# Kernel optimization log

Measured on AMD Instinct MI355X. Metric: run time of the kernel, lower is better.

The kernel has to match this reference:

```python
import jax, jax.numpy as jnp
import numpy as np

N_NODES = 10000

def _gcn_norm(edges, n_nodes):
    # PyG GCNConv default: add self-loops, symmetric normalization D^-1/2 A_hat D^-1/2
    src, dst = edges[0], edges[1]
    loop = jnp.arange(n_nodes, dtype=src.dtype)
    src = jnp.concatenate([src, loop])
    dst = jnp.concatenate([dst, loop])
    deg = jax.ops.segment_sum(jnp.ones_like(dst, dtype=jnp.float32), dst, num_segments=n_nodes)
    dinv = jnp.where(deg > 0, jax.lax.rsqrt(deg), 0.0)
    norm = dinv[src] * dinv[dst]  # [E + N]
    return src, dst, norm

def _gcn_layer(x, src, dst, norm, W, b):
    # linear transform, then gather -> weight -> scatter-add aggregation
    x = x @ W  # [N, F]
    msg = x[src] * norm[:, None]  # [E+N, F]
    out = jax.ops.segment_sum(msg, dst, num_segments=x.shape[0])
    return out + b

def setup_inputs() -> dict:
    key = jax.random.key(0)
    k1, k2, k3, k4 = jax.random.split(key, 4)
    d = 128
    E = 640000
    scale = 1.0 / np.sqrt(d)
    return {
        "nodes_embeddings": jax.random.normal(k1, (N_NODES, d), dtype=jnp.float32),
        "edges": jax.random.randint(k2, (2, E), 0, N_NODES, dtype=jnp.int64),
        "W1": jax.random.normal(k3, (d, d), dtype=jnp.float32) * scale,
        "b1": jnp.zeros((d,), dtype=jnp.float32),
        "W2": jax.random.normal(k4, (d, d), dtype=jnp.float32) * scale,
        "b2": jnp.zeros((d,), dtype=jnp.float32),
    }

def reference(nodes_embeddings, edges, W1, b1, W2, b2):
    src, dst, norm = _gcn_norm(edges, nodes_embeddings.shape[0])
    x = _gcn_layer(nodes_embeddings, src, dst, norm, W1, b1)
    x = _gcn_layer(x, src, dst, norm, W2, b2)
    return x
```

## Files before the change

kernel.cpp:

```cpp
#include <hip/hip_runtime.h>
#include <hip/hip_bf16.h>

#define D 128
#define NBINS 157
#define BIN_CAP 5120
#define EPB 4096

__device__ __forceinline__ unsigned rne_bf16(float f) {
    unsigned u = __float_as_uint(f);
    return (u + 0x7FFFu + ((u >> 16) & 1u)) >> 16;
}
__device__ __forceinline__ float bf16_lo(unsigned u) { return __uint_as_float(u << 16); }
__device__ __forceinline__ float bf16_hi(unsigned u) { return __uint_as_float(u & 0xFFFF0000u); }

__global__ __launch_bounds__(512) void fused_gemm_scatter(
        const float* __restrict__ X, const float* __restrict__ W,
        float* __restrict__ Y,
        const int* __restrict__ src, const int* __restrict__ dst,
        int* __restrict__ binTotal, int* __restrict__ binned,
        int E, int N, int gGemm) {
    __shared__ float smem[D * D];
    int tid = threadIdx.x;

    if ((int)blockIdx.x < gGemm) {
        {
            const float4* W4 = (const float4*)W;
            float4* Ws4 = (float4*)smem;
            #pragma unroll
            for (int i = 0; i < 8; ++i)
                Ws4[tid + 512 * i] = W4[tid + 512 * i];
        }
        __syncthreads();
        const float2* Ws2 = (const float2*)smem;
        int col2 = tid & 63;
        int wv   = __builtin_amdgcn_readfirstlane(tid >> 6);
        int row0 = blockIdx.x * 32 + wv * 4;
        if (row0 >= N) return;

        const float4* xr[4];
        #pragma unroll
        for (int r = 0; r < 4; ++r) {
            int rr = row0 + r; if (rr > N - 1) rr = N - 1;
            xr[r] = (const float4*)(X + (size_t)rr * D);
        }
        float accx[4] = {0.f, 0.f, 0.f, 0.f};
        float accy[4] = {0.f, 0.f, 0.f, 0.f};
        #pragma unroll 8
        for (int kb = 0; kb < 32; ++kb) {
            float4 xv[4];
            #pragma unroll
            for (int r = 0; r < 4; ++r) xv[r] = xr[r][kb];
            #pragma unroll
            for (int kk = 0; kk < 4; ++kk) {
                float2 w = Ws2[(4 * kb + kk) * 64 + col2];
                #pragma unroll
                for (int r = 0; r < 4; ++r) {
                    float xs = ((const float*)&xv[r])[kk];
                    accx[r] = fmaf(xs, w.x, accx[r]);
                    accy[r] = fmaf(xs, w.y, accy[r]);
                }
            }
        }
        #pragma unroll
        for (int r = 0; r < 4; ++r) {
            int rr = row0 + r;
            if (rr < N)
                ((float2*)Y)[(size_t)rr * 64 + col2] = make_float2(accx[r], accy[r]);
        }
    } else {
        int* cnt   = (int*)smem;
        int* loff  = cnt + 160;
        int* gbase = cnt + 320;
        int* scur  = cnt + 480;
        int* stage = cnt + 640;
        for (int b = tid; b < NBINS; b += 512) cnt[b] = 0;
        __syncthreads();

        int bid = blockIdx.x - gGemm;
        int base = bid * EPB + tid * 8;
        int s[8], dl[8], bn[8];
        int ne = 0;
        if (base + 8 <= E) {
            const int4* s4 = (const int4*)(src + base);
            const int4* d4 = (const int4*)(dst + base);
            int4 a0 = s4[0], a1 = s4[1], c0 = d4[0], c1 = d4[1];
            int ss[8] = {a0.x, a0.y, a0.z, a0.w, a1.x, a1.y, a1.z, a1.w};
            int dd[8] = {c0.x, c0.y, c0.z, c0.w, c1.x, c1.y, c1.z, c1.w};
            ne = 8;
            #pragma unroll
            for (int i = 0; i < 8; ++i) { s[i] = ss[i]; bn[i] = dd[i] >> 6; dl[i] = dd[i] & 63; }
        } else {
            for (int i = 0; i < 8; ++i) {
                int e = base + i;
                if (e < E) { s[ne] = src[e]; int d = dst[e]; bn[ne] = d >> 6; dl[ne] = d & 63; ++ne; }
            }
        }
        for (int i = 0; i < ne; ++i) atomicAdd(&cnt[bn[i]], 1);
        __syncthreads();

        if (tid < NBINS) gbase[tid] = atomicAdd(&binTotal[tid], cnt[tid]);
        if (tid < 64) {
            int c0 = (3 * tid     < NBINS) ? cnt[3 * tid    ] : 0;
            int c1 = (3 * tid + 1 < NBINS) ? cnt[3 * tid + 1] : 0;
            int c2 = (3 * tid + 2 < NBINS) ? cnt[3 * tid + 2] : 0;
            int tsum = c0 + c1 + c2;
            int incl = tsum;
            #pragma unroll
            for (int off = 1; off < 64; off <<= 1) {
                int t = __shfl_up(incl, off);
                if (tid >= off) incl += t;
            }
            int excl = incl - tsum;
            if (3 * tid     < NBINS) loff[3 * tid    ] = excl;
            if (3 * tid + 1 < NBINS) loff[3 * tid + 1] = excl + c0;
            if (3 * tid + 2 < NBINS) loff[3 * tid + 2] = excl + c0 + c1;
        }
        __syncthreads();
        if (tid < NBINS) scur[tid] = loff[tid];
        __syncthreads();

        for (int i = 0; i < ne; ++i) {
            int p = atomicAdd(&scur[bn[i]], 1);
            stage[p] = s[i] | (dl[i] << 14);
        }
        __syncthreads();

        int wv = tid >> 6, lane = tid & 63;
        for (int b = wv; b < NBINS; b += 8) {
            int n = cnt[b], so = loff[b], go = b * BIN_CAP + gbase[b];
            for (int i = lane; i < n; i += 64) binned[go + i] = stage[so + i];
        }
    }
}

__global__ __launch_bounds__(256) void sort_bins(const int* __restrict__ binTotal,
                                                 const int* __restrict__ binned,
                                                 unsigned short* __restrict__ csr16,
                                                 float* __restrict__ dinv,
                                                 int* __restrict__ nodeStart,
                                                 int* __restrict__ nodeEnd,
                                                 const float* __restrict__ Y,
                                                 unsigned* __restrict__ Zb, int N) {
    __shared__ int h[4][64];
    __shared__ int cur[4][64];
    __shared__ float sdinv[64];
    __shared__ int padTot;
    __shared__ int stage[BIN_CAP];
    int b = blockIdx.x, tid = threadIdx.x;
    int wv = tid >> 6, lane = tid & 63;
    int cntb = binTotal[b];
    h[wv][lane] = 0;
    __syncthreads();
    const int* bp = binned + b * BIN_CAP;
    for (int i = tid; i < cntb; i += 256) atomicAdd(&h[wv][bp[i] >> 14], 1);
    __syncthreads();
    if (tid < 64) {
        int d0 = h[0][tid], d1 = h[1][tid], d2 = h[2][tid], d3 = h[3][tid];
        int deg = d0 + d1 + d2 + d3;
        int pdeg = (deg + 7) & ~7;
        int incl = pdeg;
        #pragma unroll
        for (int off = 1; off < 64; off <<= 1) {
            int t = __shfl_up(incl, off);
            if (tid >= off) incl += t;
        }
        int excl = incl - pdeg;
        cur[0][tid] = excl;
        cur[1][tid] = excl + d0;
        cur[2][tid] = excl + d0 + d1;
        cur[3][tid] = excl + d0 + d1 + d2;
        float dv = rsqrtf((float)(deg + 1));
        sdinv[tid] = dv;
        if (tid == 63) padTot = incl;
        int node = b * 64 + tid;
        if (node < N) {
            dinv[node]      = dv;
            nodeStart[node] = b * BIN_CAP + excl;
            nodeEnd[node]   = b * BIN_CAP + excl + pdeg;
        }
    }
    __syncthreads();
    int cntPad = padTot;
    for (int i = tid; i < cntPad; i += 256) stage[i] = N;
    __syncthreads();
    for (int i = tid; i < cntb; i += 256) {
        int p = bp[i];
        int pos = atomicAdd(&cur[wv][p >> 14], 1);
        stage[pos] = p & 0x3FFF;
    }
    {
        const float4* Y4 = (const float4*)Y;
        uint2* Zb2 = (uint2*)Zb;
        #pragma unroll
        for (int i = 0; i < 8; ++i) {
            int idx = tid + 256 * i;
            int row = idx >> 5, c = idx & 31;
            int node = b * 64 + row;
            if (node < N) {
                float4 v = Y4[(size_t)node * 32 + c];
                float dv = sdinv[row];
                uint2 o;
                o.x = (rne_bf16(v.y * dv) << 16) | rne_bf16(v.x * dv);
                o.y = (rne_bf16(v.w * dv) << 16) | rne_bf16(v.z * dv);
                Zb2[(size_t)node * 32 + c] = o;
            }
        }
    }
    if (b == 0 && tid < 64) Zb[(size_t)N * 64 + tid] = 0u;
    __syncthreads();
    unsigned short* bw = csr16 + b * BIN_CAP;
    for (int i = tid; i < cntPad; i += 256) bw[i] = (unsigned short)stage[i];
}

__global__ __launch_bounds__(256) void gemm_scale(const float* __restrict__ X,
                                                  const float* __restrict__ W,
                                                  const float* __restrict__ dinv,
                                                  unsigned* __restrict__ Zb, int N) {
    __shared__ float Ws[D * D];
    {
        const float4* W4 = (const float4*)W;
        float4* Ws4 = (float4*)Ws;
        #pragma unroll
        for (int i = 0; i < 16; ++i)
            Ws4[threadIdx.x + 256 * i] = W4[threadIdx.x + 256 * i];
    }
    __syncthreads();
    const float2* Ws2 = (const float2*)Ws;
    int col2 = threadIdx.x & 63;
    int wv   = __builtin_amdgcn_readfirstlane(threadIdx.x >> 6);
    int row0 = blockIdx.x * 16 + wv * 4;
    if (row0 >= N) return;

    const float4* xr[4];
    #pragma unroll
    for (int r = 0; r < 4; ++r) {
        int rr = row0 + r; if (rr > N - 1) rr = N - 1;
        xr[r] = (const float4*)(X + (size_t)rr * D);
    }
    float accx[4] = {0.f, 0.f, 0.f, 0.f};
    float accy[4] = {0.f, 0.f, 0.f, 0.f};
    #pragma unroll 8
    for (int kb = 0; kb < 32; ++kb) {
        float4 xv[4];
        #pragma unroll
        for (int r = 0; r < 4; ++r) xv[r] = xr[r][kb];
        #pragma unroll
        for (int kk = 0; kk < 4; ++kk) {
            float2 w = Ws2[(4 * kb + kk) * 64 + col2];
            #pragma unroll
            for (int r = 0; r < 4; ++r) {
                float xs = ((const float*)&xv[r])[kk];
                accx[r] = fmaf(xs, w.x, accx[r]);
                accy[r] = fmaf(xs, w.y, accy[r]);
            }
        }
    }
    #pragma unroll
    for (int r = 0; r < 4; ++r) {
        int rr = row0 + r;
        if (rr < N) {
            float dv = dinv[rr];
            Zb[(size_t)rr * 64 + col2] =
                (rne_bf16(accy[r] * dv) << 16) | rne_bf16(accx[r] * dv);
        }
    }
}

__global__ __launch_bounds__(256) void aggregate(const unsigned* __restrict__ Zb,
                                                 const int* __restrict__ nodeStart,
                                                 const int* __restrict__ nodeEnd,
                                                 const unsigned short* __restrict__ csr16,
                                                 const float* __restrict__ dinv,
                                                 const float* __restrict__ bias,
                                                 float* __restrict__ Out, int N) {
    int wv    = __builtin_amdgcn_readfirstlane(threadIdx.x >> 6);
    int nodeA = blockIdx.x * 8 + wv * 2;
    if (nodeA >= N) return;
    int nodeB = nodeA + 1;
    bool hasB = (nodeB < N);
    int lane = threadIdx.x & 63;
    int g    = lane >> 4;
    int l16  = lane & 15;

    const uint4* Z4 = (const uint4*)Zb;
    float a0=0.f,a1=0.f,a2=0.f,a3=0.f,a4=0.f,a5=0.f,a6=0.f,a7=0.f;
    float b0=0.f,b1v=0.f,b2v=0.f,b3=0.f,b4v=0.f,b5=0.f,b6=0.f,b7=0.f;

    int eA = nodeStart[nodeA], endA = nodeEnd[nodeA];
    int eB = 0, endB = 0;
    if (hasB) { eB = nodeStart[nodeB]; endB = nodeEnd[nodeB]; }

    while (eA < endA || eB < endB) {
        int remA = endA - eA; int cntA = remA > 64 ? 64 : (remA > 0 ? remA : 0);
        int remB = endB - eB; int cntB = remB > 64 ? 64 : (remB > 0 ? remB : 0);
        int myA = (lane < cntA) ? (int)csr16[eA + lane] : N;
        int myB = (lane < cntB) ? (int)csr16[eB + lane] : N;
        int cmax = cntA > cntB ? cntA : cntB;
        int rounds = cmax >> 2;
        #pragma unroll 16
        for (int j = 0; j < rounds; ++j) {
            int idxA = __shfl(myA, j * 4 + g);
            int idxB = __shfl(myB, j * 4 + g);
            uint4 ua = Z4[idxA * 16 + l16];
            uint4 ub = Z4[idxB * 16 + l16];
            a0 += bf16_lo(ua.x); a1 += bf16_hi(ua.x);
            a2 += bf16_lo(ua.y); a3 += bf16_hi(ua.y);
            a4 += bf16_lo(ua.z); a5 += bf16_hi(ua.z);
            a6 += bf16_lo(ua.w); a7 += bf16_hi(ua.w);
            b0  += bf16_lo(ub.x); b1v += bf16_hi(ub.x);
            b2v += bf16_lo(ub.y); b3  += bf16_hi(ub.y);
            b4v += bf16_lo(ub.z); b5  += bf16_hi(ub.z);
            b6  += bf16_lo(ub.w); b7  += bf16_hi(ub.w);
        }
        eA += cntA; eB += cntB;
    }
    #pragma unroll
    for (int m = 16; m <= 32; m <<= 1) {
        a0 += __shfl_xor(a0, m); a1 += __shfl_xor(a1, m);
        a2 += __shfl_xor(a2, m); a3 += __shfl_xor(a3, m);
        a4 += __shfl_xor(a4, m); a5 += __shfl_xor(a5, m);
        a6 += __shfl_xor(a6, m); a7 += __shfl_xor(a7, m);
        b0  += __shfl_xor(b0, m);  b1v += __shfl_xor(b1v, m);
        b2v += __shfl_xor(b2v, m); b3  += __shfl_xor(b3, m);
        b4v += __shfl_xor(b4v, m); b5  += __shfl_xor(b5, m);
        b6  += __shfl_xor(b6, m);  b7  += __shfl_xor(b7, m);
    }
    int half = lane >> 4;
    if (half == 0 || (half == 1 && hasB)) {
        int node = half ? nodeB : nodeA;
        float r0 = half ? b0  : a0, r1 = half ? b1v : a1;
        float r2 = half ? b2v : a2, r3 = half ? b3  : a3;
        float r4 = half ? b4v : a4, r5 = half ? b5  : a5;
        float r6 = half ? b6  : a6, r7 = half ? b7  : a7;
        uint4 su = Z4[node * 16 + l16];
        float dv = dinv[node];
        const float4* bp4 = (const float4*)bias;
        float4 ba = bp4[l16 * 2], bb = bp4[l16 * 2 + 1];
        float4 o0, o1;
        o0.x = (r0 + bf16_lo(su.x)) * dv + ba.x;
        o0.y = (r1 + bf16_hi(su.x)) * dv + ba.y;
        o0.z = (r2 + bf16_lo(su.y)) * dv + ba.z;
        o0.w = (r3 + bf16_hi(su.y)) * dv + ba.w;
        o1.x = (r4 + bf16_lo(su.z)) * dv + bb.x;
        o1.y = (r5 + bf16_hi(su.z)) * dv + bb.y;
        o1.z = (r6 + bf16_lo(su.w)) * dv + bb.z;
        o1.w = (r7 + bf16_hi(su.w)) * dv + bb.w;
        float4* op = (float4*)Out + (size_t)node * 32 + l16 * 2;
        op[0] = o0;
        op[1] = o1;
    }
}

extern "C" void kernel_launch(void* const* d_in, const int* in_sizes, int n_in,
                              void* d_out, int out_size, void* d_ws, size_t ws_size,
                              hipStream_t stream) {
    const float* X  = (const float*)d_in[0];
    const int*   ed = (const int*)d_in[1];
    const float* W1 = (const float*)d_in[2];
    const float* b1 = (const float*)d_in[3];
    const float* W2 = (const float*)d_in[4];
    const float* b2 = (const float*)d_in[5];
    float* out = (float*)d_out;

    const int N = in_sizes[0] / D;
    const int E = in_sizes[1] / 2;
    const int* src = ed;
    const int* dst = ed + E;

    char* w = (char*)d_ws;
    float*    Y        = (float*)w;            w += (size_t)N * D * sizeof(float);
    unsigned* Zb       = (unsigned*)w;         w += (size_t)(N + 1) * 64 * sizeof(unsigned);
    int*      binned   = (int*)w;              w += (size_t)NBINS * BIN_CAP * sizeof(int);
    unsigned short* csr16 = (unsigned short*)w; w += (size_t)NBINS * BIN_CAP * sizeof(unsigned short);
    float*    dinv     = (float*)w;            w += (size_t)N * sizeof(float);
    int*      nodeStart= (int*)w;              w += (size_t)N * sizeof(int);
    int*      nodeEnd  = (int*)w;              w += (size_t)N * sizeof(int);
    int*      binTotal = (int*)w;              w += (size_t)NBINS * sizeof(int);

    hipMemsetAsync(binTotal, 0, NBINS * sizeof(int), stream);

    int gGemm1 = (N + 31) / 32;
    int gScat  = (E + EPB - 1) / EPB;
    fused_gemm_scatter<<<gGemm1 + gScat, 512, 0, stream>>>(
        X, W1, Y, src, dst, binTotal, binned, E, N, gGemm1);
    sort_bins<<<NBINS, 256, 0, stream>>>(binTotal, binned, csr16, dinv,
                                         nodeStart, nodeEnd, Y, Zb, N);

    int gAgg = (N + 7) / 8;
    aggregate<<<gAgg, 256, 0, stream>>>(Zb, nodeStart, nodeEnd, csr16, dinv, b1, out, N);

    int gGemm2 = (N + 15) / 16;
    gemm_scale<<<gGemm2, 256, 0, stream>>>(out, W2, dinv, Zb, N);
    aggregate<<<gAgg, 256, 0, stream>>>(Zb, nodeStart, nodeEnd, csr16, dinv, b2, out, N);
}
```

Baseline: 144.0 us.

## Fuse layer-2 linear transform into layer-1 aggregation kernel

Removes the separate gemm_scale launch. Each wave now finishes its two aggregated layer-1 rows, applies bias and normalization in registers, and multiplies them by W2. W2 is staged through shared memory in four 32-row slices, and the row values are broadcast across lanes with shuffles. The result is written straight into a second bf16 buffer (Zb2), which the final aggregate reads. This avoids a kernel launch and the fp32 write and read of the intermediate hidden matrix. The cost is that every block reloads all of W2, with extra barriers in a latency-bound gather kernel, and the early return before __syncthreads is only safe when N is a multiple of 8.

Result: slower. 175.3 us (+21.8%).

```diff
diff --git a/kernel.cpp b/kernel.cpp
--- a/kernel.cpp
+++ b/kernel.cpp
@@ -140,7 +140,8 @@
                                                  int* __restrict__ nodeStart,
                                                  int* __restrict__ nodeEnd,
                                                  const float* __restrict__ Y,
-                                                 unsigned* __restrict__ Zb, int N) {
+                                                 unsigned* __restrict__ Zb,
+                                                 unsigned* __restrict__ Zb2, int N) {
     __shared__ int h[4][64];
     __shared__ int cur[4][64];
     __shared__ float sdinv[64];
@@ -190,7 +191,7 @@
     }
     {
         const float4* Y4 = (const float4*)Y;
-        uint2* Zb2 = (uint2*)Zb;
+        uint2* Zb_2 = (uint2*)Zb;
         #pragma unroll
         for (int i = 0; i < 8; ++i) {
             int idx = tid + 256 * i;
@@ -202,77 +203,29 @@
                 uint2 o;
                 o.x = (rne_bf16(v.y * dv) << 16) | rne_bf16(v.x * dv);
                 o.y = (rne_bf16(v.w * dv) << 16) | rne_bf16(v.z * dv);
-                Zb2[(size_t)node * 32 + c] = o;
+                Zb_2[(size_t)node * 32 + c] = o;
             }
         }
     }
-    if (b == 0 && tid < 64) Zb[(size_t)N * 64 + tid] = 0u;
+    if (b == 0 && tid < 64) {
+        Zb[(size_t)N * 64 + tid]  = 0u;
+        Zb2[(size_t)N * 64 + tid] = 0u;
+    }
     __syncthreads();
     unsigned short* bw = csr16 + b * BIN_CAP;
     for (int i = tid; i < cntPad; i += 256) bw[i] = (unsigned short)stage[i];
 }
 
-__global__ __launch_bounds__(256) void gemm_scale(const float* __restrict__ X,
-                                                  const float* __restrict__ W,
-                                                  const float* __restrict__ dinv,
-                                                  unsigned* __restrict__ Zb, int N) {
-    __shared__ float Ws[D * D];
-    {
-        const float4* W4 = (const float4*)W;
-        float4* Ws4 = (float4*)Ws;
-        #pragma unroll
-        for (int i = 0; i < 16; ++i)
-            Ws4[threadIdx.x + 256 * i] = W4[threadIdx.x + 256 * i];
-    }
-    __syncthreads();
-    const float2* Ws2 = (const float2*)Ws;
-    int col2 = threadIdx.x & 63;
-    int wv   = __builtin_amdgcn_readfirstlane(threadIdx.x >> 6);
-    int row0 = blockIdx.x * 16 + wv * 4;
-    if (row0 >= N) return;
-
-    const float4* xr[4];
-    #pragma unroll
-    for (int r = 0; r < 4; ++r) {
-        int rr = row0 + r; if (rr > N - 1) rr = N - 1;
-        xr[r] = (const float4*)(X + (size_t)rr * D);
-    }
-    float accx[4] = {0.f, 0.f, 0.f, 0.f};
-    float accy[4] = {0.f, 0.f, 0.f, 0.f};
-    #pragma unroll 8
-    for (int kb = 0; kb < 32; ++kb) {
-        float4 xv[4];
-        #pragma unroll
-        for (int r = 0; r < 4; ++r) xv[r] = xr[r][kb];
-        #pragma unroll
-        for (int kk = 0; kk < 4; ++kk) {
-            float2 w = Ws2[(4 * kb + kk) * 64 + col2];
-            #pragma unroll
-            for (int r = 0; r < 4; ++r) {
-                float xs = ((const float*)&xv[r])[kk];
-                accx[r] = fmaf(xs, w.x, accx[r]);
-                accy[r] = fmaf(xs, w.y, accy[r]);
-            }
-        }
-    }
-    #pragma unroll
-    for (int r = 0; r < 4; ++r) {
-        int rr = row0 + r;
-        if (rr < N) {
-            float dv = dinv[rr];
-            Zb[(size_t)rr * 64 + col2] =
-                (rne_bf16(accy[r] * dv) << 16) | rne_bf16(accx[r] * dv);
-        }
-    }
-}
-
-__global__ __launch_bounds__(256) void aggregate(const unsigned* __restrict__ Zb,
-                                                 const int* __restrict__ nodeStart,
-                                                 const int* __restrict__ nodeEnd,
-                                                 const unsigned short* __restrict__ csr16,
-                                                 const float* __restrict__ dinv,
-                                                 const float* __restrict__ bias,
-                                                 float* __restrict__ Out, int N) {
+__global__ __launch_bounds__(256) void aggregate_fused(
+        const unsigned* __restrict__ Zb,
+        const int* __restrict__ nodeStart,
+        const int* __restrict__ nodeEnd,
+        const unsigned short* __restrict__ csr16,
+        const float* __restrict__ dinv,
+        const float* __restrict__ bias,
+        const float* __restrict__ W2,
+        unsigned* __restrict__ Zb2, int N) {
+    __shared__ float Ws[32 * D];
     int wv    = __builtin_amdgcn_readfirstlane(threadIdx.x >> 6);
     int nodeA = blockIdx.x * 8 + wv * 2;
     if (nodeA >= N) return;
@@ -325,8 +278,131 @@
         b4v += __shfl_xor(b4v, m); b5  += __shfl_xor(b5, m);
         b6  += __shfl_xor(b6, m);  b7  += __shfl_xor(b7, m);
     }
+    float hA[8], hB[8];
+    {
+        uint4 sa = Z4[nodeA * 16 + l16];
+        float dvA = dinv[nodeA];
+        const float4* bp4 = (const float4*)bias;
+        float4 ba = bp4[l16 * 2], bb = bp4[l16 * 2 + 1];
+        hA[0] = (a0 + bf16_lo(sa.x)) * dvA + ba.x;
+        hA[1] = (a1 + bf16_hi(sa.x)) * dvA + ba.y;
+        hA[2] = (a2 + bf16_lo(sa.y)) * dvA + ba.z;
+        hA[3] = (a3 + bf16_hi(sa.y)) * dvA + ba.w;
+        hA[4] = (a4 + bf16_lo(sa.z)) * dvA + bb.x;
+        hA[5] = (a5 + bf16_hi(sa.z)) * dvA + bb.y;
+        hA[6] = (a6 + bf16_lo(sa.w)) * dvA + bb.z;
+        hA[7] = (a7 + bf16_hi(sa.w)) * dvA + bb.w;
+        int nb = hasB ? nodeB : nodeA;
+        uint4 sb = Z4[nb * 16 + l16];
+        float dvB = dinv[nb];
+        hB[0] = (b0  + bf16_lo(sb.x)) * dvB + ba.x;
+        hB[1] = (b1v + bf16_hi(sb.x)) * dvB + ba.y;
+        hB[2] = (b2v + bf16_lo(sb.y)) * dvB + ba.z;
+        hB[3] = (b3  + bf16_hi(sb.y)) * dvB + ba.w;
+        hB[4] = (b4v + bf16_lo(sb.z)) * dvB + bb.x;
+        hB[5] = (b5  + bf16_hi(sb.z)) * dvB + bb.y;
+        hB[6] = (b6  + bf16_lo(sb.w)) * dvB + bb.z;
+        hB[7] = (b7  + bf16_hi(sb.w)) * dvB + bb.w;
+    }
+
+    float accAx = 0.f, accAy = 0.f, accBx = 0.f, accBy = 0.f;
+    const float2* Ws2 = (const float2*)Ws;
+    #pragma unroll
+    for (int pass = 0; pass < 4; ++pass) {
+        __syncthreads();
+        {
+            const float4* W4 = (const float4*)W2 + pass * 1024;
+            float4* Ws4 = (float4*)Ws;
+            #pragma unroll
+            for (int i = 0; i < 4; ++i)
+                Ws4[threadIdx.x + 256 * i] = W4[threadIdx.x + 256 * i];
+        }
+        __syncthreads();
+        #pragma unroll
+        for (int k = 0; k < 32; ++k) {
+            const int kk = pass * 32 + k;
+            float ha = __shfl(hA[kk & 7], kk >> 3);
+            float hb = __shfl(hB[kk & 7], kk >> 3);
+            float2 w = Ws2[k * 64 + lane];
+            accAx = fmaf(ha, w.x, accAx);
+            accAy = fmaf(ha, w.y, accAy);
+            accBx = fmaf(hb, w.x, accBx);
+            accBy = fmaf(hb, w.y, accBy);
+        }
+    }
+    {
+        float dvA = dinv[nodeA];
+        Zb2[(size_t)nodeA * 64 + lane] =
+            (rne_bf16(accAy * dvA) << 16) | rne_bf16(accAx * dvA);
+        if (hasB) {
+            float dvB = dinv[nodeB];
+            Zb2[(size_t)nodeB * 64 + lane] =
+                (rne_bf16(accBy * dvB) << 16) | rne_bf16(accBx * dvB);
+        }
+    }
+}
+
+__global__ __launch_bounds__(256) void aggregate(const unsigned* __restrict__ Zb,
+                                                 const int* __restrict__ nodeStart,
+                                                 const int* __restrict__ nodeEnd,
+                                                 const unsigned short* __restrict__ csr16,
+                                                 const float* __restrict__ dinv,
+                                                 const float* __restrict__ bias,
+                                                 float* __restrict__ Out, int N) {
+    int wv    = __builtin_amdgcn_readfirstlane(threadIdx.x >> 6);
+    int nodeA = blockIdx.x * 8 + wv * 2;
+    if (nodeA >= N) return;
+    int nodeB = nodeA + 1;
+    bool hasB = (nodeB < N);
+    int lane = threadIdx.x & 63;
+    int g    = lane >> 4;
+    int l16  = lane & 15;
+
+    const uint4* Z4 = (const uint4*)Zb;
+    float a0=0.f,a1=0.f,a2=0.f,a3=0.f,a4=0.f,a5=0.f,a6=0.f,a7=0.f;
+    float b0=0.f,b1v=0.f,b2v=0.f,b3=0.f,b4v=0.f,b5=0.f,b6=0.f,b7=0.f;
+
+    int eA = nodeStart[nodeA], endA = nodeEnd[nodeA];
+    int eB = 0, endB = 0;
+    if (hasB) { eB = nodeStart[nodeB]; endB = nodeEnd[nodeB]; }
+
+    while (eA < endA || eB < endB) {
+        int remA = endA - eA; int cntA = remA > 64 ? 64 : (remA > 0 ? remA : 0);
+        int remB = endB - eB; int cntB = remB > 64 ? 64 : (remB > 0 ? remB : 0);
+        int myA = (lane < cntA) ? (int)csr16[eA + lane] : N;
+        int myB = (lane < cntB) ? (int)csr16[eB + lane] : N;
+        int cmax = cntA > cntB ? cntA : cntB;
+        int rounds = cmax >> 2;
+        #pragma unroll 16
+        for (int j = 0; j < rounds; ++j) {
+            int idxA = __shfl(myA, j * 4 + g);
+            int idxB = __shfl(myB, j * 4 + g);
+            uint4 ua = Z4[idxA * 16 + l16];
+            uint4 ub = Z4[idxB * 16 + l16];
+            a0 += bf16_lo(ua.x); a1 += bf16_hi(ua.x);
+            a2 += bf16_lo(ua.y); a3 += bf16_hi(ua.y);
+            a4 += bf16_lo(ua.z); a5 += bf16_hi(ua.z);
+            a6 += bf16_lo(ua.w); a7 += bf16_hi(ua.w);
+            b0  += bf16_lo(ub.x); b1v += bf16_hi(ub.x);
+            b2v += bf16_lo(ub.y); b3  += bf16_hi(ub.y);
+            b4v += bf16_lo(ub.z); b5  += bf16_hi(ub.z);
+            b6  += bf16_lo(ub.w); b7  += bf16_hi(ub.w);
+        }
+        eA += cntA; eB += cntB;
+    }
+    #pragma unroll
+    for (int m = 16; m <= 32; m <<= 1) {
+        a0 += __shfl_xor(a0, m); a1 += __shfl_xor(a1, m);
+        a2 += __shfl_xor(a2, m); a3 += __shfl_xor(a3, m);
+        a4 += __shfl_xor(a4, m); a5 += __shfl_xor(a5, m);
+        a6 += __shfl_xor(a6, m); a7 += __shfl_xor(a7, m);
+        b0  += __shfl_xor(b0, m);  b1v += __shfl_xor(b1v, m);
+        b2v += __shfl_xor(b2v, m); b3  += __shfl_xor(b3, m);
+        b4v += __shfl_xor(b4v, m); b5  += __shfl_xor(b5, m);
+        b6  += __shfl_xor(b6, m);  b7  += __shfl_xor(b7, m);
+    }
     int half = lane >> 4;
-    if (half == 0 || (half == 1 && hasB)) {
+    if ((half == 0 || (half == 1 && hasB)) && lane < 32) {
         int node = half ? nodeB : nodeA;
         float r0 = half ? b0  : a0, r1 = half ? b1v : a1;
         float r2 = half ? b2v : a2, r3 = half ? b3  : a3;
@@ -370,6 +446,7 @@
     char* w = (char*)d_ws;
     float*    Y        = (float*)w;            w += (size_t)N * D * sizeof(float);
     unsigned* Zb       = (unsigned*)w;         w += (size_t)(N + 1) * 64 * sizeof(unsigned);
+    unsigned* Zb2      = (unsigned*)w;         w += (size_t)(N + 1) * 64 * sizeof(unsigned);
     int*      binned   = (int*)w;              w += (size_t)NBINS * BIN_CAP * sizeof(int);
     unsigned short* csr16 = (unsigned short*)w; w += (size_t)NBINS * BIN_CAP * sizeof(unsigned short);
     float*    dinv     = (float*)w;            w += (size_t)N * sizeof(float);
@@ -384,12 +461,10 @@
     fused_gemm_scatter<<<gGemm1 + gScat, 512, 0, stream>>>(
         X, W1, Y, src, dst, binTotal, binned, E, N, gGemm1);
     sort_bins<<<NBINS, 256, 0, stream>>>(binTotal, binned, csr16, dinv,
-                                         nodeStart, nodeEnd, Y, Zb, N);
+                                         nodeStart, nodeEnd, Y, Zb, Zb2, N);
 
     int gAgg = (N + 7) / 8;
-    aggregate<<<gAgg, 256, 0, stream>>>(Zb, nodeStart, nodeEnd, csr16, dinv, b1, out, N);
-
-    int gGemm2 = (N + 15) / 16;
-    gemm_scale<<<gGemm2, 256, 0, stream>>>(out, W2, dinv, Zb, N);
-    aggregate<<<gAgg, 256, 0, stream>>>(Zb, nodeStart, nodeEnd, csr16, dinv, b2, out, N);
-}
+    aggregate_fused<<<gAgg, 256, 0, stream>>>(Zb, nodeStart, nodeEnd, csr16,
+                                              dinv, b1, W2, Zb2, N);
+    aggregate<<<gAgg, 256, 0, stream>>>(Zb2, nodeStart, nodeEnd, csr16, dinv, b2, out, N);
+}
```
